# Performance work log

Hardware: AMD Instinct MI355X
Metric: run time of the kernel (lower is better)

The kernel has to match this reference:

```python
import jax, jax.numpy as jnp
import numpy as np

B, CQ, CKV, H, W = 16, 512, 512, 48, 48
NH = 8
HD = CQ // NH
SCALE = HD ** -0.5


def setup_inputs() -> dict:
    key = jax.random.key(0)
    ks = jax.random.split(key, 11)
    s = 0.02
    return {
        "query_features": jax.random.normal(ks[0], (B, CQ, H, W), jnp.float32),
        "key_features": jax.random.normal(ks[1], (B, CKV, H, W), jnp.float32),
        "value_features": jax.random.normal(ks[2], (B, CKV, H, W), jnp.float32),
        "Wq": jax.random.normal(ks[3], (CQ, CQ), jnp.float32) * s,
        "bq": jnp.zeros((CQ,), jnp.float32),
        "Wk": jax.random.normal(ks[4], (CQ, CKV), jnp.float32) * s,
        "bk": jnp.zeros((CQ,), jnp.float32),
        "Wv": jax.random.normal(ks[5], (CQ, CKV), jnp.float32) * s,
        "bv": jnp.zeros((CQ,), jnp.float32),
        "Wo": jax.random.normal(ks[6], (CQ, CQ), jnp.float32) * s,
        "bo": jnp.zeros((CQ,), jnp.float32),
    }


def _proj(x, Wt, b):
    # 1x1 conv == channel GEMM: (O,C) x (B,C,H,W) -> (B,O,H,W)
    return jnp.einsum('oc,bchw->bohw', Wt, x) + b[None, :, None, None]


def reference(query_features, key_features, value_features,
              Wq, bq, Wk, bk, Wv, bv, Wo, bo):
    b, cq, h, w = query_features.shape
    hw = h * w
    Q = _proj(query_features, Wq, bq).reshape(b, NH, HD, hw)
    K = _proj(key_features, Wk, bk).reshape(b, NH, HD, hw)
    V = _proj(value_features, Wv, bv).reshape(b, NH, HD, hw)
    # NOTE: faithful to source — contraction is over the SPATIAL axis d=H*W,
    # so scores are (B, NH, HD, HD) (head_dim x head_dim attention).
    scores = jnp.einsum('bnhd,bnkd->bnhk', Q, K) * SCALE
    attn = jax.nn.softmax(scores, axis=-1)
    out = jnp.einsum('bnhk,bnkd->bnhd', attn, V)  # (B, NH, HD, HW)
    out = out.reshape(b, cq, h, w)
    return _proj(out, Wo, bo)
```

## Files before the change

kernel.cpp:

```cpp
#include <hip/hip_runtime.h>
#include <hip/hip_bf16.h>

#define B_   16
#define C_   512
#define HW_  2304
#define NH_  8
#define HD_  64
#define SCALE_ 0.125f

typedef __bf16 bf16x8 __attribute__((ext_vector_type(8)));
typedef __bf16 bf16x4 __attribute__((ext_vector_type(4)));
typedef __bf16 bf16x2 __attribute__((ext_vector_type(2)));
typedef float  f32x4  __attribute__((ext_vector_type(4)));

#define MFMA16(a, b, c) __builtin_amdgcn_mfma_f32_16x16x32_bf16((a), (b), (c), 0, 0, 0)

__global__ __launch_bounds__(256) void proj_qkv(
    const float* __restrict__ qf, const float* __restrict__ kf, const float* __restrict__ vf,
    const float* __restrict__ Wq, const float* __restrict__ Wk, const float* __restrict__ Wv,
    const float* __restrict__ bq, const float* __restrict__ bk, const float* __restrict__ bv,
    __bf16* __restrict__ ws)
{
    const int z = blockIdx.z;
    const int p = z >> 4;
    const int b = z & 15;
    const float* X;
    const float* W;
    const float* bias;
    if (p == 0)      { X = qf; W = Wq; bias = bq; }
    else if (p == 1) { X = kf; W = Wk; bias = bk; }
    else             { X = vf; W = Wv; bias = bv; }
    __bf16* Y = ws + (size_t)p * ((size_t)B_ * C_ * HW_)
                   + (size_t)b * C_ * HW_;
    X += (size_t)b * C_ * HW_;

    const int n0 = blockIdx.x * 128;
    const int m0 = blockIdx.y * 128;

    __shared__ __align__(16) __bf16 As[128 * 40];
    __shared__ __align__(16) __bf16 Bs[64 * 72];

    const int t    = threadIdx.x;
    const int w    = t >> 6;
    const int lane = t & 63;
    const int l16  = lane & 15;
    const int q    = lane >> 4;
    const int wm   = w >> 1;
    const int wn   = w & 1;

    const int mA = t >> 1;
    const int kA = (t & 1) * 16;
    const int mB = t & 63;
    const int kB = (t >> 6) * 8;

    f32x4 acc[4][4] = {};

    for (int ks = 0; ks < 16; ++ks) {
        const int k0 = ks * 32;
        __syncthreads();
        {
            const float* src = W + (size_t)(m0 + mA) * 512 + k0 + kA;
            const float4 f0 = *(const float4*)(src + 0);
            const float4 f1 = *(const float4*)(src + 4);
            const float4 f2 = *(const float4*)(src + 8);
            const float4 f3 = *(const float4*)(src + 12);
            bf16x8 v0, v1;
            v0[0] = (__bf16)f0.x; v0[1] = (__bf16)f0.y; v0[2] = (__bf16)f0.z; v0[3] = (__bf16)f0.w;
            v0[4] = (__bf16)f1.x; v0[5] = (__bf16)f1.y; v0[6] = (__bf16)f1.z; v0[7] = (__bf16)f1.w;
            v1[0] = (__bf16)f2.x; v1[1] = (__bf16)f2.y; v1[2] = (__bf16)f2.z; v1[3] = (__bf16)f2.w;
            v1[4] = (__bf16)f3.x; v1[5] = (__bf16)f3.y; v1[6] = (__bf16)f3.z; v1[7] = (__bf16)f3.w;
            *(bf16x8*)&As[mA * 40 + kA]     = v0;
            *(bf16x8*)&As[mA * 40 + kA + 8] = v1;
        }
        {
            bf16x8 r0, r1;
            #pragma unroll
            for (int j = 0; j < 8; ++j) {
                const float2 v = *(const float2*)&X[(size_t)(k0 + kB + j) * HW_ + n0 + 2 * mB];
                r0[j] = (__bf16)v.x;
                r1[j] = (__bf16)v.y;
            }
            *(bf16x8*)&Bs[mB * 72 + kB]      = r0;
            *(bf16x8*)&Bs[mB * 72 + 32 + kB] = r1;
        }
        __syncthreads();
        bf16x8 af[4], bfr[4];
        #pragma unroll
        for (int mi = 0; mi < 4; ++mi)
            af[mi] = *(bf16x8*)&As[(wm * 64 + mi * 16 + l16) * 40 + q * 8];
        #pragma unroll
        for (int ni = 0; ni < 4; ++ni) {
            const int n = wn * 64 + ni * 16 + l16;
            bfr[ni] = *(bf16x8*)&Bs[(n >> 1) * 72 + (n & 1) * 32 + q * 8];
        }
        #pragma unroll
        for (int mi = 0; mi < 4; ++mi)
            #pragma unroll
            for (int ni = 0; ni < 4; ++ni)
                acc[mi][ni] = MFMA16(af[mi], bfr[ni], acc[mi][ni]);
    }

    #pragma unroll
    for (int mi = 0; mi < 4; ++mi) {
        #pragma unroll
        for (int r = 0; r < 4; ++r) {
            const int m = m0 + wm * 64 + mi * 16 + q * 4 + r;
            const float bv_ = bias[m];
            #pragma unroll
            for (int ni = 0; ni < 4; ++ni) {
                const int n = n0 + wn * 64 + ni * 16 + l16;
                Y[(size_t)m * HW_ + n] = (__bf16)(acc[mi][ni][r] + bv_);
            }
        }
    }
}

__global__ __launch_bounds__(256) void attn_scores(
    const __bf16* __restrict__ Qw, const __bf16* __restrict__ Kw, __bf16* __restrict__ Pw)
{
    const int bn = blockIdx.x;
    const __bf16* Qb = Qw + (size_t)bn * 64 * HW_;
    const __bf16* Kb = Kw + (size_t)bn * 64 * HW_;

    __shared__ __align__(16) __bf16 Qs[64 * 72];
    __shared__ __align__(16) __bf16 Ks[64 * 72];

    const int t    = threadIdx.x;
    const int w    = t >> 6;
    const int lane = t & 63;
    const int l16  = lane & 15;
    const int q    = lane >> 4;
    const int row  = t >> 2;
    const int kc   = (t & 3) * 16;

    f32x4 acc[4] = {};

    for (int it = 0; it < 36; ++it) {
        const int k0 = it * 64;
        __syncthreads();
        *(bf16x8*)&Qs[row * 72 + kc]     = *(const bf16x8*)&Qb[(size_t)row * HW_ + k0 + kc];
        *(bf16x8*)&Qs[row * 72 + kc + 8] = *(const bf16x8*)&Qb[(size_t)row * HW_ + k0 + kc + 8];
        *(bf16x8*)&Ks[row * 72 + kc]     = *(const bf16x8*)&Kb[(size_t)row * HW_ + k0 + kc];
        *(bf16x8*)&Ks[row * 72 + kc + 8] = *(const bf16x8*)&Kb[(size_t)row * HW_ + k0 + kc + 8];
        __syncthreads();
        #pragma unroll
        for (int kk = 0; kk < 2; ++kk) {
            const bf16x8 a = *(bf16x8*)&Qs[(w * 16 + l16) * 72 + kk * 32 + q * 8];
            #pragma unroll
            for (int ni = 0; ni < 4; ++ni) {
                const bf16x8 bb = *(bf16x8*)&Ks[(ni * 16 + l16) * 72 + kk * 32 + q * 8];
                acc[ni] = MFMA16(a, bb, acc[ni]);
            }
        }
    }

    #pragma unroll
    for (int ni = 0; ni < 4; ++ni)
        #pragma unroll
        for (int r = 0; r < 4; ++r)
            acc[ni][r] *= SCALE_;

    #pragma unroll
    for (int r = 0; r < 4; ++r) {
        float mx = fmaxf(fmaxf(acc[0][r], acc[1][r]), fmaxf(acc[2][r], acc[3][r]));
        mx = fmaxf(mx, __shfl_xor(mx, 1));
        mx = fmaxf(mx, __shfl_xor(mx, 2));
        mx = fmaxf(mx, __shfl_xor(mx, 4));
        mx = fmaxf(mx, __shfl_xor(mx, 8));
        float s = 0.f;
        #pragma unroll
        for (int ni = 0; ni < 4; ++ni) {
            const float e = expf(acc[ni][r] - mx);
            acc[ni][r] = e;
            s += e;
        }
        s += __shfl_xor(s, 1);
        s += __shfl_xor(s, 2);
        s += __shfl_xor(s, 4);
        s += __shfl_xor(s, 8);
        const float inv = 1.f / s;
        #pragma unroll
        for (int ni = 0; ni < 4; ++ni)
            acc[ni][r] *= inv;
    }

    #pragma unroll
    for (int r = 0; r < 4; ++r)
        #pragma unroll
        for (int ni = 0; ni < 4; ++ni)
            Pw[(size_t)bn * 4096 + (w * 16 + q * 4 + r) * 64 + ni * 16 + l16] =
                (__bf16)acc[ni][r];
}

__global__ __launch_bounds__(256) void attn_pv(
    const __bf16* __restrict__ Pw, const __bf16* __restrict__ Vw, __bf16* __restrict__ AO)
{
    const int dsl = blockIdx.x;
    const int bn  = blockIdx.y;
    const int t    = threadIdx.x;
    const int w    = t >> 6;
    const int lane = t & 63;
    const int l16  = lane & 15;
    const int q    = lane >> 4;

    __shared__ __align__(16) __bf16 Ps[64 * 72];
    __shared__ __align__(16) __bf16 Vt[4][16 * 264];

    {
        const int row = t >> 2;
        const int kc  = (t & 3) * 16;
        *(bf16x8*)&Ps[row * 72 + kc]     = *(const bf16x8*)&Pw[(size_t)bn * 4096 + row * 64 + kc];
        *(bf16x8*)&Ps[row * 72 + kc + 8] = *(const bf16x8*)&Pw[(size_t)bn * 4096 + row * 64 + kc + 8];
    }

    const __bf16* Vb = Vw + (size_t)bn * 64 * HW_;
    const int d0w = dsl * 256 + w * 64;
    {
        const int m4 = lane & 15;
        const int kh = (lane >> 4) * 16;
        __bf16 rr[4][16];
        #pragma unroll
        for (int j = 0; j < 16; ++j) {
            const bf16x4 v = *(const bf16x4*)&Vb[(size_t)(kh + j) * HW_ + d0w + 4 * m4];
            #pragma unroll
            for (int e = 0; e < 4; ++e) rr[e][j] = v[e];
        }
        #pragma unroll
        for (int e = 0; e < 4; ++e) {
            bf16x8 s0, s1;
            #pragma unroll
            for (int j = 0; j < 8; ++j) { s0[j] = rr[e][j]; s1[j] = rr[e][8 + j]; }
            *(bf16x8*)&Vt[w][m4 * 264 + e * 64 + kh]     = s0;
            *(bf16x8*)&Vt[w][m4 * 264 + e * 64 + kh + 8] = s1;
        }
    }
    __syncthreads();

    f32x4 acc[4][4] = {};
    #pragma unroll
    for (int kk = 0; kk < 2; ++kk) {
        bf16x8 af[4], bfr[4];
        #pragma unroll
        for (int mi = 0; mi < 4; ++mi)
            af[mi] = *(bf16x8*)&Ps[(mi * 16 + l16) * 72 + kk * 32 + q * 8];
        #pragma unroll
        for (int ni = 0; ni < 4; ++ni) {
            const int dl = ni * 16 + l16;
            bfr[ni] = *(bf16x8*)&Vt[w][(dl >> 2) * 264 + (dl & 3) * 64 + kk * 32 + q * 8];
        }
        #pragma unroll
        for (int mi = 0; mi < 4; ++mi)
            #pragma unroll
            for (int ni = 0; ni < 4; ++ni)
                acc[mi][ni] = MFMA16(af[mi], bfr[ni], acc[mi][ni]);
    }

    #pragma unroll
    for (int mi = 0; mi < 4; ++mi)
        #pragma unroll
        for (int r = 0; r < 4; ++r) {
            const int m = mi * 16 + q * 4 + r;
            #pragma unroll
            for (int ni = 0; ni < 4; ++ni) {
                const int d = d0w + ni * 16 + l16;
                AO[((size_t)bn * 64 + m) * HW_ + d] = (__bf16)acc[mi][ni][r];
            }
        }
}

__global__ __launch_bounds__(256) void proj_out(
    const __bf16* __restrict__ AO, const float* __restrict__ Wo, const float* __restrict__ bo,
    float* __restrict__ out)
{
    const int b  = blockIdx.z;
    const int n0 = blockIdx.x * 128;
    const int m0 = blockIdx.y * 128;
    const __bf16* Xb = AO + (size_t)b * C_ * HW_;
    float* Yb = out + (size_t)b * C_ * HW_;

    __shared__ __align__(16) __bf16 As[128 * 40];
    __shared__ __align__(16) __bf16 Bs[64 * 72];

    const int t    = threadIdx.x;
    const int w    = t >> 6;
    const int lane = t & 63;
    const int l16  = lane & 15;
    const int q    = lane >> 4;
    const int wm   = w >> 1;
    const int wn   = w & 1;

    const int mA = t >> 1;
    const int kA = (t & 1) * 16;
    const int mB = t & 63;
    const int kB = (t >> 6) * 8;

    f32x4 acc[4][4] = {};

    for (int ks = 0; ks < 16; ++ks) {
        const int k0 = ks * 32;
        __syncthreads();
        {
            const float* src = Wo + (size_t)(m0 + mA) * 512 + k0 + kA;
            const float4 f0 = *(const float4*)(src + 0);
            const float4 f1 = *(const float4*)(src + 4);
            const float4 f2 = *(const float4*)(src + 8);
            const float4 f3 = *(const float4*)(src + 12);
            bf16x8 v0, v1;
            v0[0] = (__bf16)f0.x; v0[1] = (__bf16)f0.y; v0[2] = (__bf16)f0.z; v0[3] = (__bf16)f0.w;
            v0[4] = (__bf16)f1.x; v0[5] = (__bf16)f1.y; v0[6] = (__bf16)f1.z; v0[7] = (__bf16)f1.w;
            v1[0] = (__bf16)f2.x; v1[1] = (__bf16)f2.y; v1[2] = (__bf16)f2.z; v1[3] = (__bf16)f2.w;
            v1[4] = (__bf16)f3.x; v1[5] = (__bf16)f3.y; v1[6] = (__bf16)f3.z; v1[7] = (__bf16)f3.w;
            *(bf16x8*)&As[mA * 40 + kA]     = v0;
            *(bf16x8*)&As[mA * 40 + kA + 8] = v1;
        }
        {
            bf16x8 r0, r1;
            #pragma unroll
            for (int j = 0; j < 8; ++j) {
                const bf16x2 v = *(const bf16x2*)&Xb[(size_t)(k0 + kB + j) * HW_ + n0 + 2 * mB];
                r0[j] = v[0];
                r1[j] = v[1];
            }
            *(bf16x8*)&Bs[mB * 72 + kB]      = r0;
            *(bf16x8*)&Bs[mB * 72 + 32 + kB] = r1;
        }
        __syncthreads();
        bf16x8 af[4], bfr[4];
        #pragma unroll
        for (int mi = 0; mi < 4; ++mi)
            af[mi] = *(bf16x8*)&As[(wm * 64 + mi * 16 + l16) * 40 + q * 8];
        #pragma unroll
        for (int ni = 0; ni < 4; ++ni) {
            const int n = wn * 64 + ni * 16 + l16;
            bfr[ni] = *(bf16x8*)&Bs[(n >> 1) * 72 + (n & 1) * 32 + q * 8];
        }
        #pragma unroll
        for (int mi = 0; mi < 4; ++mi)
            #pragma unroll
            for (int ni = 0; ni < 4; ++ni)
                acc[mi][ni] = MFMA16(af[mi], bfr[ni], acc[mi][ni]);
    }

    #pragma unroll
    for (int mi = 0; mi < 4; ++mi) {
        #pragma unroll
        for (int r = 0; r < 4; ++r) {
            const int m = m0 + wm * 64 + mi * 16 + q * 4 + r;
            const float bias = bo[m];
            #pragma unroll
            for (int ni = 0; ni < 4; ++ni) {
                const int n = n0 + wn * 64 + ni * 16 + l16;
                Yb[(size_t)m * HW_ + n] = acc[mi][ni][r] + bias;
            }
        }
    }
}

extern "C" void kernel_launch(void* const* d_in, const int* in_sizes, int n_in,
                              void* d_out, int out_size, void* d_ws, size_t ws_size,
                              hipStream_t stream)
{
    (void)in_sizes; (void)n_in; (void)out_size; (void)ws_size;
    const float* qf = (const float*)d_in[0];
    const float* kf = (const float*)d_in[1];
    const float* vf = (const float*)d_in[2];
    const float* Wq = (const float*)d_in[3];
    const float* bq = (const float*)d_in[4];
    const float* Wk = (const float*)d_in[5];
    const float* bk = (const float*)d_in[6];
    const float* Wv = (const float*)d_in[7];
    const float* bv = (const float*)d_in[8];
    const float* Wo = (const float*)d_in[9];
    const float* bo = (const float*)d_in[10];

    const size_t QE = (size_t)B_ * C_ * HW_;
    __bf16* Qw = (__bf16*)d_ws;
    __bf16* Kw = Qw + QE;
    __bf16* Vw = Qw + 2 * QE;
    __bf16* AO = Qw + 3 * QE;
    __bf16* Pw = Qw + 4 * QE;

    proj_qkv   <<<dim3(18, 4, 48), 256, 0, stream>>>(qf, kf, vf, Wq, Wk, Wv, bq, bk, bv, Qw);
    attn_scores<<<dim3(128),       256, 0, stream>>>(Qw, Kw, Pw);
    attn_pv    <<<dim3(9, 128),    256, 0, stream>>>(Pw, Vw, AO);
    proj_out   <<<dim3(18, 4, 16), 256, 0, stream>>>(AO, Wo, bo, (float*)d_out);
}
```

Baseline: 489.4 us.

## Pre-transpose activations to bf16, use direct-to-LDS loads, split-K the score GEMM

Adds a transpose-and-convert kernel that turns fp32 channel-major inputs into bf16 spatial-major tiles. The projection GEMMs can then stream B tiles with global_load_lds 16-byte copies instead of strided float2 gathers, and they use a K-step of 64. The score GEMM is split along the spatial axis into 6 partial blocks, with a separate kernel that sums the partials and applies softmax, which raises parallelism from 128 blocks. attn_pv now writes its output transposed so proj_out uses the same direct-load path. The cost is extra kernel launches, an extra pass over the inputs for the transpose, and a reused workspace region.

New measurement: 488.4 us. About the same (-0.2%).

```diff
diff --git a/kernel.cpp b/kernel.cpp
--- a/kernel.cpp
+++ b/kernel.cpp
@@ -10,94 +10,109 @@
 
 typedef __bf16 bf16x8 __attribute__((ext_vector_type(8)));
 typedef __bf16 bf16x4 __attribute__((ext_vector_type(4)));
-typedef __bf16 bf16x2 __attribute__((ext_vector_type(2)));
 typedef float  f32x4  __attribute__((ext_vector_type(4)));
 
 #define MFMA16(a, b, c) __builtin_amdgcn_mfma_f32_16x16x32_bf16((a), (b), (c), 0, 0, 0)
 
-__global__ __launch_bounds__(256) void proj_qkv(
-    const float* __restrict__ qf, const float* __restrict__ kf, const float* __restrict__ vf,
-    const float* __restrict__ Wq, const float* __restrict__ Wk, const float* __restrict__ Wv,
-    const float* __restrict__ bq, const float* __restrict__ bk, const float* __restrict__ bv,
-    __bf16* __restrict__ ws)
-{
-    const int z = blockIdx.z;
-    const int p = z >> 4;
-    const int b = z & 15;
-    const float* X;
-    const float* W;
-    const float* bias;
-    if (p == 0)      { X = qf; W = Wq; bias = bq; }
-    else if (p == 1) { X = kf; W = Wk; bias = bk; }
-    else             { X = vf; W = Wv; bias = bv; }
-    __bf16* Y = ws + (size_t)p * ((size_t)B_ * C_ * HW_)
-                   + (size_t)b * C_ * HW_;
-    X += (size_t)b * C_ * HW_;
-
+__device__ __forceinline__ void gload_lds16(const void* g, void* l) {
+    __builtin_amdgcn_global_load_lds(
+        (const __attribute__((address_space(1))) unsigned int*)g,
+        (__attribute__((address_space(3))) unsigned int*)l, 16, 0, 0);
+}
+
+__global__ __launch_bounds__(256) void transpose_cvt(
+    const float* __restrict__ X, __bf16* __restrict__ XT)
+{
+    const int b  = blockIdx.z;
+    const int c0 = blockIdx.y * 64;
+    const int h0 = blockIdx.x * 128;
+    const float* Xb = X + (size_t)b * C_ * HW_;
+    __bf16* XTb = XT + (size_t)b * HW_ * C_;
+
+    __shared__ float Ts[64 * 129];
+    const int t = threadIdx.x;
+
+    #pragma unroll
+    for (int p = 0; p < 8; ++p) {
+        const int c  = p * 8 + (t >> 5);
+        const int hg = (t & 31) * 4;
+        const float4 v = *(const float4*)&Xb[(size_t)(c0 + c) * HW_ + h0 + hg];
+        Ts[c * 129 + hg + 0] = v.x;
+        Ts[c * 129 + hg + 1] = v.y;
+        Ts[c * 129 + hg + 2] = v.z;
+        Ts[c * 129 + hg + 3] = v.w;
+    }
+    __syncthreads();
+    #pragma unroll
+    for (int p = 0; p < 4; ++p) {
+        const int hw = p * 32 + (t >> 3);
+        const int g  = (t & 7) * 8;
+        bf16x8 o;
+        #pragma unroll
+        for (int e = 0; e < 8; ++e)
+            o[e] = (__bf16)Ts[(g + e) * 129 + hw];
+        *(bf16x8*)&XTb[(size_t)(h0 + hw) * C_ + c0 + g] = o;
+    }
+}
+
+__global__ __launch_bounds__(256) void proj_gemm(
+    const __bf16* __restrict__ XT, const float* __restrict__ W,
+    const float* __restrict__ bias, __bf16* __restrict__ Y)
+{
+    const int b  = blockIdx.z;
     const int n0 = blockIdx.x * 128;
     const int m0 = blockIdx.y * 128;
-
-    __shared__ __align__(16) __bf16 As[128 * 40];
-    __shared__ __align__(16) __bf16 Bs[64 * 72];
-
-    const int t    = threadIdx.x;
-    const int w    = t >> 6;
-    const int lane = t & 63;
-    const int l16  = lane & 15;
-    const int q    = lane >> 4;
-    const int wm   = w >> 1;
-    const int wn   = w & 1;
-
-    const int mA = t >> 1;
-    const int kA = (t & 1) * 16;
-    const int mB = t & 63;
-    const int kB = (t >> 6) * 8;
+    const __bf16* XTb = XT + (size_t)b * HW_ * C_;
+    __bf16* Yb = Y + (size_t)b * C_ * HW_;
+
+    __shared__ __align__(16) __bf16 As[128 * 64];
+    __shared__ __align__(16) __bf16 Bs[128 * 64];
+
+    const int t = threadIdx.x;
+    const int w = t >> 6, lane = t & 63, l16 = lane & 15, q = lane >> 4;
+    const int wm = w >> 1, wn = w & 1;
+
+    const int ar = t >> 4;
+    const int ak = (t & 15) * 4;
+    const int br = lane >> 3;
+    const int bg = (lane & 7) * 8;
 
     f32x4 acc[4][4] = {};
 
-    for (int ks = 0; ks < 16; ++ks) {
-        const int k0 = ks * 32;
-        __syncthreads();
-        {
-            const float* src = W + (size_t)(m0 + mA) * 512 + k0 + kA;
-            const float4 f0 = *(const float4*)(src + 0);
-            const float4 f1 = *(const float4*)(src + 4);
-            const float4 f2 = *(const float4*)(src + 8);
-            const float4 f3 = *(const float4*)(src + 12);
-            bf16x8 v0, v1;
-            v0[0] = (__bf16)f0.x; v0[1] = (__bf16)f0.y; v0[2] = (__bf16)f0.z; v0[3] = (__bf16)f0.w;
-            v0[4] = (__bf16)f1.x; v0[5] = (__bf16)f1.y; v0[6] = (__bf16)f1.z; v0[7] = (__bf16)f1.w;
-            v1[0] = (__bf16)f2.x; v1[1] = (__bf16)f2.y; v1[2] = (__bf16)f2.z; v1[3] = (__bf16)f2.w;
-            v1[4] = (__bf16)f3.x; v1[5] = (__bf16)f3.y; v1[6] = (__bf16)f3.z; v1[7] = (__bf16)f3.w;
-            *(bf16x8*)&As[mA * 40 + kA]     = v0;
-            *(bf16x8*)&As[mA * 40 + kA + 8] = v1;
-        }
-        {
-            bf16x8 r0, r1;
-            #pragma unroll
-            for (int j = 0; j < 8; ++j) {
-                const float2 v = *(const float2*)&X[(size_t)(k0 + kB + j) * HW_ + n0 + 2 * mB];
-                r0[j] = (__bf16)v.x;
-                r1[j] = (__bf16)v.y;
-            }
-            *(bf16x8*)&Bs[mB * 72 + kB]      = r0;
-            *(bf16x8*)&Bs[mB * 72 + 32 + kB] = r1;
-        }
-        __syncthreads();
-        bf16x8 af[4], bfr[4];
-        #pragma unroll
-        for (int mi = 0; mi < 4; ++mi)
-            af[mi] = *(bf16x8*)&As[(wm * 64 + mi * 16 + l16) * 40 + q * 8];
-        #pragma unroll
-        for (int ni = 0; ni < 4; ++ni) {
-            const int n = wn * 64 + ni * 16 + l16;
-            bfr[ni] = *(bf16x8*)&Bs[(n >> 1) * 72 + (n & 1) * 32 + q * 8];
-        }
-        #pragma unroll
-        for (int mi = 0; mi < 4; ++mi)
+    for (int ks = 0; ks < 8; ++ks) {
+        const int k0 = ks * 64;
+        __syncthreads();
+        #pragma unroll
+        for (int pb = 0; pb < 4; ++pb) {
+            const int rbase = pb * 32 + w * 8;
+            gload_lds16(&XTb[(size_t)(n0 + rbase + br) * C_ + k0 + bg],
+                        &Bs[rbase * 64]);
+        }
+        #pragma unroll
+        for (int pa = 0; pa < 8; ++pa) {
+            const int row = pa * 16 + ar;
+            const float4 f = *(const float4*)&W[(size_t)(m0 + row) * C_ + k0 + ak];
+            bf16x4 v;
+            v[0] = (__bf16)f.x; v[1] = (__bf16)f.y;
+            v[2] = (__bf16)f.z; v[3] = (__bf16)f.w;
+            *(bf16x4*)&As[row * 64 + ak] = v;
+        }
+        __syncthreads();
+        #pragma unroll
+        for (int kk = 0; kk < 2; ++kk) {
+            bf16x8 af[4], bfr[4];
+            #pragma unroll
+            for (int mi = 0; mi < 4; ++mi)
+                af[mi] = *(bf16x8*)&As[(wm * 64 + mi * 16 + l16) * 64 + kk * 32 + q * 8];
             #pragma unroll
             for (int ni = 0; ni < 4; ++ni)
-                acc[mi][ni] = MFMA16(af[mi], bfr[ni], acc[mi][ni]);
+                bfr[ni] = *(bf16x8*)&Bs[(wn * 64 + ni * 16 + l16) * 64 + kk * 32 + q * 8];
+            #pragma unroll
+            for (int mi = 0; mi < 4; ++mi)
+                #pragma unroll
+                for (int ni = 0; ni < 4; ++ni)
+                    acc[mi][ni] = MFMA16(af[mi], bfr[ni], acc[mi][ni]);
+        }
     }
 
     #pragma unroll
@@ -109,16 +124,18 @@
             #pragma unroll
             for (int ni = 0; ni < 4; ++ni) {
                 const int n = n0 + wn * 64 + ni * 16 + l16;
-                Y[(size_t)m * HW_ + n] = (__bf16)(acc[mi][ni][r] + bv_);
+                Yb[(size_t)m * HW_ + n] = (__bf16)(acc[mi][ni][r] + bv_);
             }
         }
     }
 }
 
-__global__ __launch_bounds__(256) void attn_scores(
-    const __bf16* __restrict__ Qw, const __bf16* __restrict__ Kw, __bf16* __restrict__ Pw)
-{
-    const int bn = blockIdx.x;
+__global__ __launch_bounds__(256) void attn_scores_part(
+    const __bf16* __restrict__ Qw, const __bf16* __restrict__ Kw,
+    float* __restrict__ Sp)
+{
+    const int bn  = blockIdx.x;
+    const int kcs = blockIdx.y;
     const __bf16* Qb = Qw + (size_t)bn * 64 * HW_;
     const __bf16* Kb = Kw + (size_t)bn * 64 * HW_;
 
@@ -135,8 +152,8 @@
 
     f32x4 acc[4] = {};
 
-    for (int it = 0; it < 36; ++it) {
-        const int k0 = it * 64;
+    for (int it = 0; it < 6; ++it) {
+        const int k0 = kcs * 384 + it * 64;
         __syncthreads();
         *(bf16x8*)&Qs[row * 72 + kc]     = *(const bf16x8*)&Qb[(size_t)row * HW_ + k0 + kc];
         *(bf16x8*)&Qs[row * 72 + kc + 8] = *(const bf16x8*)&Qb[(size_t)row * HW_ + k0 + kc + 8];
@@ -154,46 +171,59 @@
         }
     }
 
-    #pragma unroll
-    for (int ni = 0; ni < 4; ++ni)
-        #pragma unroll
-        for (int r = 0; r < 4; ++r)
-            acc[ni][r] *= SCALE_;
-
-    #pragma unroll
-    for (int r = 0; r < 4; ++r) {
-        float mx = fmaxf(fmaxf(acc[0][r], acc[1][r]), fmaxf(acc[2][r], acc[3][r]));
-        mx = fmaxf(mx, __shfl_xor(mx, 1));
-        mx = fmaxf(mx, __shfl_xor(mx, 2));
-        mx = fmaxf(mx, __shfl_xor(mx, 4));
-        mx = fmaxf(mx, __shfl_xor(mx, 8));
-        float s = 0.f;
-        #pragma unroll
-        for (int ni = 0; ni < 4; ++ni) {
-            const float e = expf(acc[ni][r] - mx);
-            acc[ni][r] = e;
-            s += e;
-        }
-        s += __shfl_xor(s, 1);
-        s += __shfl_xor(s, 2);
-        s += __shfl_xor(s, 4);
-        s += __shfl_xor(s, 8);
-        const float inv = 1.f / s;
+    float* S = Sp + ((size_t)kcs * 128 + bn) * 4096;
+    #pragma unroll
+    for (int r = 0; r < 4; ++r)
         #pragma unroll
         for (int ni = 0; ni < 4; ++ni)
-            acc[ni][r] *= inv;
-    }
-
-    #pragma unroll
-    for (int r = 0; r < 4; ++r)
-        #pragma unroll
-        for (int ni = 0; ni < 4; ++ni)
-            Pw[(size_t)bn * 4096 + (w * 16 + q * 4 + r) * 64 + ni * 16 + l16] =
-                (__bf16)acc[ni][r];
+            S[(w * 16 + q * 4 + r) * 64 + ni * 16 + l16] = acc[ni][r];
+}
+
+__global__ __launch_bounds__(256) void softmax_reduce(
+    const float* __restrict__ Sp, __bf16* __restrict__ Pw)
+{
+    const int bn = blockIdx.x;
+    const int t  = threadIdx.x;
+    const int r  = t >> 2;
+    const int c0 = (t & 3) * 16;
+
+    float v[16];
+    #pragma unroll
+    for (int j = 0; j < 16; ++j) v[j] = 0.f;
+    #pragma unroll
+    for (int kc = 0; kc < 6; ++kc) {
+        const float* s = Sp + ((size_t)kc * 128 + bn) * 4096 + r * 64 + c0;
+        #pragma unroll
+        for (int j4 = 0; j4 < 4; ++j4) {
+            const float4 f = *(const float4*)&s[j4 * 4];
+            v[j4 * 4 + 0] += f.x; v[j4 * 4 + 1] += f.y;
+            v[j4 * 4 + 2] += f.z; v[j4 * 4 + 3] += f.w;
+        }
+    }
+    float mx = -1e30f;
+    #pragma unroll
+    for (int j = 0; j < 16; ++j) { v[j] *= SCALE_; mx = fmaxf(mx, v[j]); }
+    mx = fmaxf(mx, __shfl_xor(mx, 1));
+    mx = fmaxf(mx, __shfl_xor(mx, 2));
+    float s = 0.f;
+    #pragma unroll
+    for (int j = 0; j < 16; ++j) { v[j] = __expf(v[j] - mx); s += v[j]; }
+    s += __shfl_xor(s, 1);
+    s += __shfl_xor(s, 2);
+    const float inv = 1.f / s;
+    bf16x8 o0, o1;
+    #pragma unroll
+    for (int j = 0; j < 8; ++j) {
+        o0[j] = (__bf16)(v[j] * inv);
+        o1[j] = (__bf16)(v[8 + j] * inv);
+    }
+    *(bf16x8*)&Pw[(size_t)bn * 4096 + r * 64 + c0]     = o0;
+    *(bf16x8*)&Pw[(size_t)bn * 4096 + r * 64 + c0 + 8] = o1;
 }
 
 __global__ __launch_bounds__(256) void attn_pv(
-    const __bf16* __restrict__ Pw, const __bf16* __restrict__ Vw, __bf16* __restrict__ AO)
+    const __bf16* __restrict__ Pw, const __bf16* __restrict__ Vw,
+    __bf16* __restrict__ AOT)
 {
     const int dsl = blockIdx.x;
     const int bn  = blockIdx.y;
@@ -255,90 +285,78 @@
                 acc[mi][ni] = MFMA16(af[mi], bfr[ni], acc[mi][ni]);
     }
 
+    const int bb = bn >> 3;
+    const int nh = bn & 7;
     #pragma unroll
     for (int mi = 0; mi < 4; ++mi)
         #pragma unroll
-        for (int r = 0; r < 4; ++r) {
-            const int m = mi * 16 + q * 4 + r;
-            #pragma unroll
-            for (int ni = 0; ni < 4; ++ni) {
-                const int d = d0w + ni * 16 + l16;
-                AO[((size_t)bn * 64 + m) * HW_ + d] = (__bf16)acc[mi][ni][r];
-            }
+        for (int ni = 0; ni < 4; ++ni) {
+            const int d = d0w + ni * 16 + l16;
+            bf16x4 o;
+            #pragma unroll
+            for (int r = 0; r < 4; ++r) o[r] = (__bf16)acc[mi][ni][r];
+            *(bf16x4*)&AOT[((size_t)bb * HW_ + d) * C_ + nh * 64 + mi * 16 + q * 4] = o;
         }
 }
 
 __global__ __launch_bounds__(256) void proj_out(
-    const __bf16* __restrict__ AO, const float* __restrict__ Wo, const float* __restrict__ bo,
-    float* __restrict__ out)
+    const __bf16* __restrict__ AOT, const float* __restrict__ W,
+    const float* __restrict__ bias, float* __restrict__ out)
 {
     const int b  = blockIdx.z;
     const int n0 = blockIdx.x * 128;
     const int m0 = blockIdx.y * 128;
-    const __bf16* Xb = AO + (size_t)b * C_ * HW_;
+    const __bf16* XTb = AOT + (size_t)b * HW_ * C_;
     float* Yb = out + (size_t)b * C_ * HW_;
 
-    __shared__ __align__(16) __bf16 As[128 * 40];
-    __shared__ __align__(16) __bf16 Bs[64 * 72];
-
-    const int t    = threadIdx.x;
-    const int w    = t >> 6;
-    const int lane = t & 63;
-    const int l16  = lane & 15;
-    const int q    = lane >> 4;
-    const int wm   = w >> 1;
-    const int wn   = w & 1;
-
-    const int mA = t >> 1;
-    const int kA = (t & 1) * 16;
-    const int mB = t & 63;
-    const int kB = (t >> 6) * 8;
+    __shared__ __align__(16) __bf16 As[128 * 64];
+    __shared__ __align__(16) __bf16 Bs[128 * 64];
+
+    const int t = threadIdx.x;
+    const int w = t >> 6, lane = t & 63, l16 = lane & 15, q = lane >> 4;
+    const int wm = w >> 1, wn = w & 1;
+
+    const int ar = t >> 4;
+    const int ak = (t & 15) * 4;
+    const int br = lane >> 3;
+    const int bg = (lane & 7) * 8;
 
     f32x4 acc[4][4] = {};
 
-    for (int ks = 0; ks < 16; ++ks) {
-        const int k0 = ks * 32;
-        __syncthreads();
-        {
-            const float* src = Wo + (size_t)(m0 + mA) * 512 + k0 + kA;
-            const float4 f0 = *(const float4*)(src + 0);
-            const float4 f1 = *(const float4*)(src + 4);
-            const float4 f2 = *(const float4*)(src + 8);
-            const float4 f3 = *(const float4*)(src + 12);
-            bf16x8 v0, v1;
-            v0[0] = (__bf16)f0.x; v0[1] = (__bf16)f0.y; v0[2] = (__bf16)f0.z; v0[3] = (__bf16)f0.w;
-            v0[4] = (__bf16)f1.x; v0[5] = (__bf16)f1.y; v0[6] = (__bf16)f1.z; v0[7] = (__bf16)f1.w;
-            v1[0] = (__bf16)f2.x; v1[1] = (__bf16)f2.y; v1[2] = (__bf16)f2.z; v1[3] = (__bf16)f2.w;
-            v1[4] = (__bf16)f3.x; v1[5] = (__bf16)f3.y; v1[6] = (__bf16)f3.z; v1[7] = (__bf16)f3.w;
-            *(bf16x8*)&As[mA * 40 + kA]     = v0;
-            *(bf16x8*)&As[mA * 40 + kA + 8] = v1;
-        }
-        {
-            bf16x8 r0, r1;
-            #pragma unroll
-            for (int j = 0; j < 8; ++j) {
-                const bf16x2 v = *(const bf16x2*)&Xb[(size_t)(k0 + kB + j) * HW_ + n0 + 2 * mB];
-                r0[j] = v[0];
-                r1[j] = v[1];
-            }
-            *(bf16x8*)&Bs[mB * 72 + kB]      = r0;
-            *(bf16x8*)&Bs[mB * 72 + 32 + kB] = r1;
-        }
-        __syncthreads();
-        bf16x8 af[4], bfr[4];
-        #pragma unroll
-        for (int mi = 0; mi < 4; ++mi)
-            af[mi] = *(bf16x8*)&As[(wm * 64 + mi * 16 + l16) * 40 + q * 8];
-        #pragma unroll
-        for (int ni = 0; ni < 4; ++ni) {
-            const int n = wn * 64 + ni * 16 + l16;
-            bfr[ni] = *(bf16x8*)&Bs[(n >> 1) * 72 + (n & 1) * 32 + q * 8];
-        }
-        #pragma unroll
-        for (int mi = 0; mi < 4; ++mi)
+    for (int ks = 0; ks < 8; ++ks) {
+        const int k0 = ks * 64;
+        __syncthreads();
+        #pragma unroll
+        for (int pb = 0; pb < 4; ++pb) {
+            const int rbase = pb * 32 + w * 8;
+            gload_lds16(&XTb[(size_t)(n0 + rbase + br) * C_ + k0 + bg],
+                        &Bs[rbase * 64]);
+        }
+        #pragma unroll
+        for (int pa = 0; pa < 8; ++pa) {
+            const int row = pa * 16 + ar;
+            const float4 f = *(const float4*)&W[(size_t)(m0 + row) * C_ + k0 + ak];
+            bf16x4 v;
+            v[0] = (__bf16)f.x; v[1] = (__bf16)f.y;
+            v[2] = (__bf16)f.z; v[3] = (__bf16)f.w;
+            *(bf16x4*)&As[row * 64 + ak] = v;
+        }
+        __syncthreads();
+        #pragma unroll
+        for (int kk = 0; kk < 2; ++kk) {
+            bf16x8 af[4], bfr[4];
+            #pragma unroll
+            for (int mi = 0; mi < 4; ++mi)
+                af[mi] = *(bf16x8*)&As[(wm * 64 + mi * 16 + l16) * 64 + kk * 32 + q * 8];
             #pragma unroll
             for (int ni = 0; ni < 4; ++ni)
-                acc[mi][ni] = MFMA16(af[mi], bfr[ni], acc[mi][ni]);
+                bfr[ni] = *(bf16x8*)&Bs[(wn * 64 + ni * 16 + l16) * 64 + kk * 32 + q * 8];
+            #pragma unroll
+            for (int mi = 0; mi < 4; ++mi)
+                #pragma unroll
+                for (int ni = 0; ni < 4; ++ni)
+                    acc[mi][ni] = MFMA16(af[mi], bfr[ni], acc[mi][ni]);
+        }
     }
 
     #pragma unroll
@@ -346,11 +364,11 @@
         #pragma unroll
         for (int r = 0; r < 4; ++r) {
             const int m = m0 + wm * 64 + mi * 16 + q * 4 + r;
-            const float bias = bo[m];
+            const float bv_ = bias[m];
             #pragma unroll
             for (int ni = 0; ni < 4; ++ni) {
                 const int n = n0 + wn * 64 + ni * 16 + l16;
-                Yb[(size_t)m * HW_ + n] = acc[mi][ni][r] + bias;
+                Yb[(size_t)m * HW_ + n] = acc[mi][ni][r] + bv_;
             }
         }
     }
@@ -374,14 +392,24 @@
     const float* bo = (const float*)d_in[10];
 
     const size_t QE = (size_t)B_ * C_ * HW_;
-    __bf16* Qw = (__bf16*)d_ws;
-    __bf16* Kw = Qw + QE;
-    __bf16* Vw = Qw + 2 * QE;
-    __bf16* AO = Qw + 3 * QE;
-    __bf16* Pw = Qw + 4 * QE;
-
-    proj_qkv   <<<dim3(18, 4, 48), 256, 0, stream>>>(qf, kf, vf, Wq, Wk, Wv, bq, bk, bv, Qw);
-    attn_scores<<<dim3(128),       256, 0, stream>>>(Qw, Kw, Pw);
-    attn_pv    <<<dim3(9, 128),    256, 0, stream>>>(Pw, Vw, AO);
-    proj_out   <<<dim3(18, 4, 16), 256, 0, stream>>>(AO, Wo, bo, (float*)d_out);
-}
+    __bf16* region0 = (__bf16*)d_ws;
+    __bf16* XT  = region0;
+    float*  Sp  = (float*)region0;
+    __bf16* AOT = region0;
+    __bf16* Qw  = region0 + QE;
+    __bf16* Kw  = Qw + QE;
+    __bf16* Vw  = Kw + QE;
+    __bf16* Pw  = Vw + QE;
+
+    transpose_cvt<<<dim3(18, 8, 16), 256, 0, stream>>>(qf, XT);
+    proj_gemm    <<<dim3(18, 4, 16), 256, 0, stream>>>(XT, Wq, bq, Qw);
+    transpose_cvt<<<dim3(18, 8, 16), 256, 0, stream>>>(kf, XT);
+    proj_gemm    <<<dim3(18, 4, 16), 256, 0, stream>>>(XT, Wk, bk, Kw);
+    transpose_cvt<<<dim3(18, 8, 16), 256, 0, stream>>>(vf, XT);
+    proj_gemm    <<<dim3(18, 4, 16), 256, 0, stream>>>(XT, Wv, bv, Vw);
+
+    attn_scores_part<<<dim3(128, 6), 256, 0, stream>>>(Qw, Kw, Sp);
+    softmax_reduce  <<<dim3(128),    256, 0, stream>>>(Sp, Pw);
+    attn_pv         <<<dim3(9, 128), 256, 0, stream>>>(Pw, Vw, AOT);
+    proj_out        <<<dim3(18, 4, 16), 256, 0, stream>>>(AOT, Wo, bo, (float*)d_out);
+}
```
